# Kernel tuning notes

Measured on AMD Instinct MI355X. Metric: run time of the kernel, lower is better.

The kernel has to match this reference:

```python
import jax, jax.numpy as jnp
import numpy as np
from jax import lax

WINDOW_SIZE = 11
CHANNEL = 3
SIGMA = 1.5


def _build_window():
    # 1D gaussian, normalized, then outer product -> (C, 1, k, k) depthwise kernel
    coords = jnp.arange(WINDOW_SIZE, dtype=jnp.float32) - WINDOW_SIZE // 2
    g = jnp.exp(-coords ** 2 / (2.0 * SIGMA ** 2))
    g = g / g.sum()
    w2d = jnp.outer(g, g)  # (k, k)
    return jnp.broadcast_to(w2d[None, None], (CHANNEL, 1, WINDOW_SIZE, WINDOW_SIZE))


def _dwconv(x, w):
    pad = WINDOW_SIZE // 2
    return lax.conv_general_dilated(
        x, w,
        window_strides=(1, 1),
        padding=[(pad, pad), (pad, pad)],
        dimension_numbers=("NCHW", "OIHW", "NCHW"),
        feature_group_count=CHANNEL,
    )


def setup_inputs() -> dict:
    key = jax.random.key(0)
    k1, k2 = jax.random.split(key)
    pred = jax.random.uniform(k1, (16, 3, 512, 512), dtype=jnp.float32)
    target = jax.random.uniform(k2, (16, 3, 512, 512), dtype=jnp.float32)
    return {"pred": pred, "target": target}


def reference(pred, target):
    C1, C2 = 0.01 ** 2, 0.03 ** 2
    w = _build_window().astype(pred.dtype)

    mu_x = _dwconv(pred, w)
    mu_y = _dwconv(target, w)
    mu_x_sq = mu_x * mu_x
    mu_y_sq = mu_y * mu_y
    mu_xy = mu_x * mu_y

    sg_x = _dwconv(pred * pred, w) - mu_x_sq
    sg_y = _dwconv(target * target, w) - mu_y_sq
    sg_xy = _dwconv(pred * target, w) - mu_xy

    ssim_map = ((2.0 * mu_xy + C1) * (2.0 * sg_xy + C2)) / (
        (mu_x_sq + mu_y_sq + C1) * (sg_x + sg_y + C2)
    )
    return 1.0 - ssim_map.mean()
```

## Files before the change

### kernel.cpp

```cpp
#include <hip/hip_runtime.h>


namespace {
constexpr int IMG   = 512;
constexpr int NCH   = 48;
constexpr int TW    = 32;
constexpr int TH    = 64;
constexpr int RSTR  = 88;
constexpr int TPX   = IMG / TW;
constexpr int TPY   = IMG / TH;
constexpr int NBLK  = TPX * TPY * NCH;
constexpr int FB    = NBLK / 256;

constexpr float Wf[11] = {
    0.00102838f, 0.00759876f, 0.03600077f, 0.10936069f, 0.21300554f,
    0.26601172f,
    0.21300554f, 0.10936069f, 0.03600077f, 0.00759876f, 0.00102838f };
}

typedef _Float16 half8 __attribute__((ext_vector_type(8)));
typedef _Float16 half4v __attribute__((ext_vector_type(4)));
typedef _Float16 h2 __attribute__((ext_vector_type(2)));
typedef float float4v __attribute__((ext_vector_type(4)));

__device__ inline float band_w(int d) {
    float v = 0.f;
    #pragma unroll
    for (int k = 0; k < 11; ++k) v = (d == k) ? Wf[k] : v;
    return v;
}

__device__ inline h2 pk(float a, float b) {
    auto v = __builtin_amdgcn_cvt_pkrtz(a, b);
    h2 r;
    __builtin_memcpy(&r, &v, sizeof(r));
    return r;
}

union H8 { half8 v; h2 p[4]; };

__global__ __launch_bounds__(256, 5) void ssim_tile_kernel(
    const float* __restrict__ pred, const float* __restrict__ tgt,
    float* __restrict__ partial)
{
    __shared__ __align__(16) _Float16 hf_t[5][TW][RSTR];
    __shared__ float wred[4];

    const int t    = threadIdx.x;
    const int w    = t >> 6;
    const int lane = t & 63;
    const int nr   = lane & 15;
    const int quad = lane >> 4;

    const int bid  = blockIdx.x;
    const int img  = bid >> 7;
    const int tile = bid & 127;
    const int txi  = tile >> 3;
    const int tyi  = tile & 7;
    const int tx   = txi * TW;
    const int ty   = tyi * TH;

    const float* __restrict__ p = pred + (size_t)img * (IMG * IMG);
    const float* __restrict__ q = tgt  + (size_t)img * (IMG * IMG);

    half8 Aband, Bband;
    #pragma unroll
    for (int jj = 0; jj < 8; ++jj) {
        int k = quad * 8 + jj;
        Aband[jj] = (_Float16)band_w(k - nr);
        Bband[jj] = (_Float16)band_w(k - nr - 3);
    }
    const float4v zf = {0.f, 0.f, 0.f, 0.f};
    const half8 z8 = {};

    for (int T = w; T < 10; T += 4) {
        const int s = T >> 1;
        const int j = T & 1;
        const int gy  = ty + 16 * s + nr - 5;
        const int gyc = min(max(gy, 0), IMG - 1);
        const int cb  = tx + 16 * j - 8 + (quad << 3);
        const int cbc = min(max(cb, 0), IMG - 8);
        const bool ok = ((unsigned)gy < (unsigned)IMG) &&
                        ((unsigned)cb <= (unsigned)(IMG - 8));
        const float* rp = p + gyc * IMG + cbc;
        const float* rq = q + gyc * IMG + cbc;
        float4 xa = *(const float4*)rp;
        float4 xb = *(const float4*)(rp + 4);
        float4 ya = *(const float4*)rq;
        float4 yb = *(const float4*)(rq + 4);

        H8 ax, ay;
        ax.p[0] = pk(xa.x, xa.y); ax.p[1] = pk(xa.z, xa.w);
        ax.p[2] = pk(xb.x, xb.y); ax.p[3] = pk(xb.z, xb.w);
        ay.p[0] = pk(ya.x, ya.y); ay.p[1] = pk(ya.z, ya.w);
        ay.p[2] = pk(yb.x, yb.y); ay.p[3] = pk(yb.z, yb.w);
        if (!ok) { ax.v = z8; ay.v = z8; }

        half8 fx  = ax.v;
        half8 fy  = ay.v;
        half8 fxx = fx * fx;
        half8 fyy = fy * fy;
        half8 fxy = fx * fy;

        float4v D[5];
        D[0] = __builtin_amdgcn_mfma_f32_16x16x32_f16(fx,  Bband, zf, 0, 0, 0);
        D[1] = __builtin_amdgcn_mfma_f32_16x16x32_f16(fy,  Bband, zf, 0, 0, 0);
        D[2] = __builtin_amdgcn_mfma_f32_16x16x32_f16(fxx, Bband, zf, 0, 0, 0);
        D[3] = __builtin_amdgcn_mfma_f32_16x16x32_f16(fyy, Bband, zf, 0, 0, 0);
        D[4] = __builtin_amdgcn_mfma_f32_16x16x32_f16(fxy, Bband, zf, 0, 0, 0);

        const int col = 16 * j + nr;
        const int r0  = 16 * s + (quad << 2);
        #pragma unroll
        for (int f = 0; f < 5; ++f) {
            h2 lo = pk(D[f][0], D[f][1]);
            h2 hi = pk(D[f][2], D[f][3]);
            half4v hh = {lo[0], lo[1], hi[0], hi[1]};
            *(half4v*)&hf_t[f][col][r0] = hh;
        }
    }
    __syncthreads();

    constexpr float C1 = 1e-4f, C2 = 9e-4f;
    float lsum = 0.f;
    for (int G = w; G < 8; G += 4) {
        const int s = G >> 1;
        const int j = G & 1;
        const int col = 16 * j + nr;
        const int rb  = 16 * s + (quad << 3);
        float4v acc[5];
        #pragma unroll
        for (int f = 0; f < 5; ++f) {
            half8 bf = *(const half8*)&hf_t[f][col][rb];
            acc[f] = __builtin_amdgcn_mfma_f32_16x16x32_f16(Aband, bf, zf, 0, 0, 0);
        }
        #pragma unroll
        for (int r = 0; r < 4; ++r) {
            float mx = acc[0][r], my = acc[1][r];
            float ex2 = acc[2][r], ey2 = acc[3][r], exy = acc[4][r];
            float mxs = mx * mx, mys = my * my, mxy = mx * my;
            float sgx  = ex2 - mxs;
            float sgy  = ey2 - mys;
            float sgxy = exy - mxy;
            float num = (2.f * mxy + C1) * (2.f * sgxy + C2);
            float den = (mxs + mys + C1) * (sgx + sgy + C2);
            lsum += num * __builtin_amdgcn_rcpf(den);
        }
    }

    #pragma unroll
    for (int off = 32; off > 0; off >>= 1)
        lsum += __shfl_down(lsum, off, 64);
    if (lane == 0) wred[w] = lsum;
    __syncthreads();
    if (t == 0) partial[bid] = wred[0] + wred[1] + wred[2] + wred[3];
}

__global__ __launch_bounds__(256) void ssim_finishA(float* __restrict__ partial)
{
    __shared__ float wred[4];
    const int t = threadIdx.x;
    float s = partial[blockIdx.x * 256 + t];
    #pragma unroll
    for (int off = 32; off > 0; off >>= 1)
        s += __shfl_down(s, off, 64);
    if ((t & 63) == 0) wred[t >> 6] = s;
    __syncthreads();
    if (t == 0) partial[blockIdx.x * 256] = wred[0] + wred[1] + wred[2] + wred[3];
}

__global__ __launch_bounds__(64) void ssim_finishB(
    const float* __restrict__ partial, float* __restrict__ out)
{
    const int t = threadIdx.x;
    float s = (t < FB) ? partial[t * 256] : 0.f;
    #pragma unroll
    for (int off = 32; off > 0; off >>= 1)
        s += __shfl_down(s, off, 64);
    if (t == 0)
        out[0] = 1.f - s * (1.f / (float)((long long)NCH * IMG * IMG));
}

extern "C" void kernel_launch(void* const* d_in, const int* in_sizes, int n_in,
                              void* d_out, int out_size, void* d_ws, size_t ws_size,
                              hipStream_t stream)
{
    const float* pred = (const float*)d_in[0];
    const float* tgt  = (const float*)d_in[1];
    float* out     = (float*)d_out;
    float* partial = (float*)d_ws;

    ssim_tile_kernel<<<NBLK, 256, 0, stream>>>(pred, tgt, partial);
    ssim_finishA<<<FB, 256, 0, stream>>>(partial);
    ssim_finishB<<<1, 64, 0, stream>>>(partial, out);
}
```

Measured before the change: 138.9 us.

## Reshape tiles to 16x128 columns and vectorize SSIM epilogue with packed float2 math

Changes the per-block tile from 32x64 to 16x128, so each block covers one 16-column strip. The horizontal pass then needs 9 row-strips instead of 10 MFMA tiles per 2048 outputs, which cuts the vertical halo overhead. The epilogue is rewritten to use float2 vector arithmetic, which may map to packed FP32 instructions, and is algebraically simplified to share terms. Occupancy is raised to 6 blocks/SM via launch bounds. The risk is more register pressure and a changed LDS footprint, with row stride 152 in place of 88.

```diff
diff --git a/kernel.cpp b/kernel.cpp
--- a/kernel.cpp
+++ b/kernel.cpp
@@ -4,9 +4,9 @@
 namespace {
 constexpr int IMG   = 512;
 constexpr int NCH   = 48;
-constexpr int TW    = 32;
-constexpr int TH    = 64;
-constexpr int RSTR  = 88;
+constexpr int TW    = 16;
+constexpr int TH    = 128;
+constexpr int RSTR  = 152;
 constexpr int TPX   = IMG / TW;
 constexpr int TPY   = IMG / TH;
 constexpr int NBLK  = TPX * TPY * NCH;
@@ -22,6 +22,7 @@
 typedef _Float16 half4v __attribute__((ext_vector_type(4)));
 typedef _Float16 h2 __attribute__((ext_vector_type(2)));
 typedef float float4v __attribute__((ext_vector_type(4)));
+typedef float float2v __attribute__((ext_vector_type(2)));
 
 __device__ inline float band_w(int d) {
     float v = 0.f;
@@ -39,7 +40,7 @@
 
 union H8 { half8 v; h2 p[4]; };
 
-__global__ __launch_bounds__(256, 5) void ssim_tile_kernel(
+__global__ __launch_bounds__(256, 6) void ssim_tile_kernel(
     const float* __restrict__ pred, const float* __restrict__ tgt,
     float* __restrict__ partial)
 {
@@ -55,8 +56,8 @@
     const int bid  = blockIdx.x;
     const int img  = bid >> 7;
     const int tile = bid & 127;
-    const int txi  = tile >> 3;
-    const int tyi  = tile & 7;
+    const int txi  = tile >> 2;
+    const int tyi  = tile & 3;
     const int tx   = txi * TW;
     const int ty   = tyi * TH;
 
@@ -73,12 +74,10 @@
     const float4v zf = {0.f, 0.f, 0.f, 0.f};
     const half8 z8 = {};
 
-    for (int T = w; T < 10; T += 4) {
-        const int s = T >> 1;
-        const int j = T & 1;
+    for (int s = w; s < 9; s += 4) {
         const int gy  = ty + 16 * s + nr - 5;
         const int gyc = min(max(gy, 0), IMG - 1);
-        const int cb  = tx + 16 * j - 8 + (quad << 3);
+        const int cb  = tx - 8 + (quad << 3);
         const int cbc = min(max(cb, 0), IMG - 8);
         const bool ok = ((unsigned)gy < (unsigned)IMG) &&
                         ((unsigned)cb <= (unsigned)(IMG - 8));
@@ -109,44 +108,50 @@
         D[3] = __builtin_amdgcn_mfma_f32_16x16x32_f16(fyy, Bband, zf, 0, 0, 0);
         D[4] = __builtin_amdgcn_mfma_f32_16x16x32_f16(fxy, Bband, zf, 0, 0, 0);
 
-        const int col = 16 * j + nr;
-        const int r0  = 16 * s + (quad << 2);
+        const int r0 = 16 * s + (quad << 2);
         #pragma unroll
         for (int f = 0; f < 5; ++f) {
             h2 lo = pk(D[f][0], D[f][1]);
             h2 hi = pk(D[f][2], D[f][3]);
             half4v hh = {lo[0], lo[1], hi[0], hi[1]};
-            *(half4v*)&hf_t[f][col][r0] = hh;
+            *(half4v*)&hf_t[f][nr][r0] = hh;
         }
     }
     __syncthreads();
 
     constexpr float C1 = 1e-4f, C2 = 9e-4f;
-    float lsum = 0.f;
-    for (int G = w; G < 8; G += 4) {
-        const int s = G >> 1;
-        const int j = G & 1;
-        const int col = 16 * j + nr;
-        const int rb  = 16 * s + (quad << 3);
+    const float2v C1v = {C1, C1};
+    const float2v C2v = {C2, C2};
+    const float2v K12 = {C1 + C2, C1 + C2};
+    float2v lsum2 = {0.f, 0.f};
+    for (int s = w; s < 8; s += 4) {
+        const int rb = 16 * s + (quad << 3);
         float4v acc[5];
         #pragma unroll
         for (int f = 0; f < 5; ++f) {
-            half8 bf = *(const half8*)&hf_t[f][col][rb];
+            half8 bf = *(const half8*)&hf_t[f][nr][rb];
             acc[f] = __builtin_amdgcn_mfma_f32_16x16x32_f16(Aband, bf, zf, 0, 0, 0);
         }
         #pragma unroll
-        for (int r = 0; r < 4; ++r) {
-            float mx = acc[0][r], my = acc[1][r];
-            float ex2 = acc[2][r], ey2 = acc[3][r], exy = acc[4][r];
-            float mxs = mx * mx, mys = my * my, mxy = mx * my;
-            float sgx  = ex2 - mxs;
-            float sgy  = ey2 - mys;
-            float sgxy = exy - mxy;
-            float num = (2.f * mxy + C1) * (2.f * sgxy + C2);
-            float den = (mxs + mys + C1) * (sgx + sgy + C2);
-            lsum += num * __builtin_amdgcn_rcpf(den);
+        for (int h = 0; h < 2; ++h) {
+            float2v mx  = {acc[0][2*h], acc[0][2*h+1]};
+            float2v my  = {acc[1][2*h], acc[1][2*h+1]};
+            float2v ex2 = {acc[2][2*h], acc[2][2*h+1]};
+            float2v ey2 = {acc[3][2*h], acc[3][2*h+1]};
+            float2v exy = {acc[4][2*h], acc[4][2*h+1]};
+            float2v P  = mx * my;
+            float2v U  = mx * mx + my * my + C1v;
+            float2v n1 = 2.f * P + C1v;
+            float2v n2 = 2.f * (exy - P) + C2v;
+            float2v num = n1 * n2;
+            float2v e1 = (ex2 + ey2) - U + K12;
+            float2v den = U * e1;
+            float2v r = {__builtin_amdgcn_rcpf(den.x),
+                         __builtin_amdgcn_rcpf(den.y)};
+            lsum2 += num * r;
         }
     }
+    float lsum = lsum2.x + lsum2.y;
 
     #pragma unroll
     for (int off = 32; off > 0; off >>= 1)
```

Result: no change. 138.3 us (-0.5%).
